# Kernel optimization log

Measured on AMD Instinct MI355X. Metric: run time of the kernel, lower is better.

Reference implementation:

```python
import jax, jax.numpy as jnp
import numpy as np

N = 50000
E = 800000
IN, HID, OUT = 64, 128, 64


def sage_conv(x, edge_index, W_l, b_l, W_r):
    # PyG SAGEConv (aggr='mean', root_weight=True):
    #   out = lin_l(mean_{j in N(i)} x_j) + lin_r(x_i)
    src, dst = edge_index[0], edge_index[1]
    msg = x[src]                                   # [E, d] gather
    agg = jax.ops.segment_sum(msg, dst, num_segments=x.shape[0])  # [N, d]
    cnt = jax.ops.segment_sum(jnp.ones((msg.shape[0],), x.dtype), dst,
                              num_segments=x.shape[0])
    mean = agg / jnp.maximum(cnt, 1.0)[:, None]
    return mean @ W_l + b_l + x @ W_r


def setup_inputs() -> dict:
    key = jax.random.key(0)
    ks = jax.random.split(key, 8)
    x = jax.random.normal(ks[0], (N, IN), dtype=jnp.float32)
    edge_index = jax.random.randint(ks[1], (2, E), 0, N, dtype=jnp.int64)
    s1 = 1.0 / np.sqrt(IN)
    s2 = 1.0 / np.sqrt(HID)
    W1_l = jax.random.uniform(ks[2], (IN, HID), jnp.float32, -s1, s1)
    W1_r = jax.random.uniform(ks[3], (IN, HID), jnp.float32, -s1, s1)
    b1 = jax.random.uniform(ks[4], (HID,), jnp.float32, -s1, s1)
    W2_l = jax.random.uniform(ks[5], (HID, OUT), jnp.float32, -s2, s2)
    W2_r = jax.random.uniform(ks[6], (HID, OUT), jnp.float32, -s2, s2)
    b2 = jax.random.uniform(ks[7], (OUT,), jnp.float32, -s2, s2)
    return {"x": x, "edge_index": edge_index,
            "W1_l": W1_l, "b1": b1, "W1_r": W1_r,
            "W2_l": W2_l, "b2": b2, "W2_r": W2_r}


def reference(x, edge_index, W1_l, b1, W1_r, W2_l, b2, W2_r):
    h = jax.nn.relu(sage_conv(x, edge_index, W1_l, b1, W1_r))
    return sage_conv(h, edge_index, W2_l, b2, W2_r)
```

## Files before the change

kernel.cpp:

```cpp
#include <hip/hip_runtime.h>


#define FMA4(acc, f, w0, w1, w2, w3)                          \
  acc.x += f.x * w0.x + f.y * w1.x + f.z * w2.x + f.w * w3.x; \
  acc.y += f.x * w0.y + f.y * w1.y + f.z * w2.y + f.w * w3.y; \
  acc.z += f.x * w0.z + f.y * w1.z + f.z * w2.z + f.w * w3.z; \
  acc.w += f.x * w0.w + f.y * w1.w + f.z * w2.w + f.w * w3.w;

__global__ __launch_bounds__(256) void k_hist(const int* __restrict__ dst,
                                              int* __restrict__ deg, int E) {
  int e = blockIdx.x * blockDim.x + threadIdx.x;
  if (e < E) atomicAdd(&deg[dst[e]], 1);
}

__global__ __launch_bounds__(256) void k_assign(const int* __restrict__ deg,
                                                int* __restrict__ rowptr,
                                                int* __restrict__ pos,
                                                int* __restrict__ total,
                                                int N) {
  int i = blockIdx.x * blockDim.x + threadIdx.x;
  if (i >= N) return;
  int r = atomicAdd(total, deg[i]);
  rowptr[i] = r;
  pos[i] = r;
}

__global__ __launch_bounds__(256) void k_fill(const int* __restrict__ src,
                                              const int* __restrict__ dst,
                                              int* __restrict__ pos,
                                              int* __restrict__ colsrc, int E) {
  int e = blockIdx.x * blockDim.x + threadIdx.x;
  if (e >= E) return;
  int slot = atomicAdd(&pos[dst[e]], 1);
  colsrc[slot] = src[e];
}

__global__ __launch_bounds__(256) void k_gather(
    const float* __restrict__ feat, const int* __restrict__ rowptr,
    const int* __restrict__ deg, const int* __restrict__ colsrc,
    const float* __restrict__ addsrc, const float* __restrict__ bias,
    float* __restrict__ dstbuf, int N) {
  int wave = threadIdx.x >> 6;
  int lane = threadIdx.x & 63;
  int node = blockIdx.x * 4 + wave;
  if (node >= N) return;
  int beg = rowptr[node];
  int d = deg[node];
  int end = beg + d;
  int eg = lane >> 4;
  int c4 = (lane & 15) << 2;
  float4 s0 = make_float4(0.f, 0.f, 0.f, 0.f);
  float4 s1 = s0;
  int e = beg + eg;
  for (; e + 4 < end; e += 8) {
    const float4 v0 =
        *reinterpret_cast<const float4*>(feat + (size_t)colsrc[e] * 64 + c4);
    const float4 v1 = *reinterpret_cast<const float4*>(
        feat + (size_t)colsrc[e + 4] * 64 + c4);
    s0.x += v0.x; s0.y += v0.y; s0.z += v0.z; s0.w += v0.w;
    s1.x += v1.x; s1.y += v1.y; s1.z += v1.z; s1.w += v1.w;
  }
  for (; e < end; e += 4) {
    const float4 v =
        *reinterpret_cast<const float4*>(feat + (size_t)colsrc[e] * 64 + c4);
    s0.x += v.x; s0.y += v.y; s0.z += v.z; s0.w += v.w;
  }
  s0.x += s1.x; s0.y += s1.y; s0.z += s1.z; s0.w += s1.w;
#pragma unroll
  for (int m = 16; m <= 32; m <<= 1) {
    s0.x += __shfl_xor(s0.x, m);
    s0.y += __shfl_xor(s0.y, m);
    s0.z += __shfl_xor(s0.z, m);
    s0.w += __shfl_xor(s0.w, m);
  }
  if (eg == 0) {
    float r = 1.f / fmaxf((float)d, 1.f);
    float4 o = make_float4(s0.x * r, s0.y * r, s0.z * r, s0.w * r);
    if (addsrc != nullptr) {
      float4 a = *(const float4*)&addsrc[(size_t)node * 64 + c4];
      float4 b = *(const float4*)&bias[c4];
      o.x += a.x + b.x;
      o.y += a.y + b.y;
      o.z += a.z + b.z;
      o.w += a.w + b.w;
    }
    *reinterpret_cast<float4*>(dstbuf + (size_t)node * 64 + c4) = o;
  }
}

__global__ __launch_bounds__(256) void k_dense1(
    const float* __restrict__ x, const float* __restrict__ mean1,
    const float* __restrict__ W1l, const float* __restrict__ b1,
    const float* __restrict__ W1r, const float* __restrict__ W2l,
    const float* __restrict__ W2r, float* __restrict__ p,
    float* __restrict__ q, int N) {
  int i0 = blockIdx.x * 32;
  int tid = threadIdx.x;
  __shared__ float smem[32 * 132];
  float(*ms)[64] = (float(*)[64])smem;
  float(*xs)[64] = (float(*)[64])(smem + 32 * 64);
  float(*hs)[132] = (float(*)[132])smem;

  for (int t = tid; t < 512; t += 256) {
    int n = t >> 4;
    int c4 = (t & 15) << 2;
    int node = i0 + n;
    float4 zm, zx;
    if (node < N) {
      zm = *(const float4*)&mean1[(size_t)node * 64 + c4];
      zx = *(const float4*)&x[(size_t)node * 64 + c4];
    } else {
      zm = make_float4(0.f, 0.f, 0.f, 0.f);
      zx = zm;
    }
    *(float4*)&ms[n][c4] = zm;
    *(float4*)&xs[n][c4] = zx;
  }
  __syncthreads();

  int jt = tid & 31;
  int j0 = jt << 2;
  int nt = tid >> 5;
  int n0 = nt << 2;
  float4 acc[4];
  {
    float4 bj = *(const float4*)&b1[j0];
    acc[0] = bj; acc[1] = bj; acc[2] = bj; acc[3] = bj;
  }
  for (int k0 = 0; k0 < 64; k0 += 4) {
    float4 wl[4], wr[4];
#pragma unroll
    for (int kk = 0; kk < 4; ++kk) {
      wl[kk] = *(const float4*)&W1l[(size_t)(k0 + kk) * 128 + j0];
      wr[kk] = *(const float4*)&W1r[(size_t)(k0 + kk) * 128 + j0];
    }
#pragma unroll
    for (int n = 0; n < 4; ++n) {
      float4 m4 = *(const float4*)&ms[n0 + n][k0];
      float4 x4 = *(const float4*)&xs[n0 + n][k0];
      FMA4(acc[n], m4, wl[0], wl[1], wl[2], wl[3]);
      FMA4(acc[n], x4, wr[0], wr[1], wr[2], wr[3]);
    }
  }
  __syncthreads();

#pragma unroll
  for (int n = 0; n < 4; ++n) {
    float4 v = acc[n];
    v.x = fmaxf(v.x, 0.f);
    v.y = fmaxf(v.y, 0.f);
    v.z = fmaxf(v.z, 0.f);
    v.w = fmaxf(v.w, 0.f);
    *(float4*)&hs[n0 + n][j0] = v;
  }
  __syncthreads();

  const float* W = (tid < 128) ? W2l : W2r;
  float* ob = (tid < 128) ? p : q;
  int t2 = tid & 127;
  int jj0 = (t2 & 15) << 2;
  int nn0 = (t2 >> 4) << 2;
  float4 pa[4];
  pa[0] = make_float4(0.f, 0.f, 0.f, 0.f);
  pa[1] = pa[0]; pa[2] = pa[0]; pa[3] = pa[0];
  for (int k0 = 0; k0 < 128; k0 += 4) {
    float4 w[4];
#pragma unroll
    for (int kk = 0; kk < 4; ++kk)
      w[kk] = *(const float4*)&W[(size_t)(k0 + kk) * 64 + jj0];
#pragma unroll
    for (int n = 0; n < 4; ++n) {
      float4 h4 = *(const float4*)&hs[nn0 + n][k0];
      FMA4(pa[n], h4, w[0], w[1], w[2], w[3]);
    }
  }
#pragma unroll
  for (int n = 0; n < 4; ++n) {
    int node = i0 + nn0 + n;
    if (node < N) *(float4*)&ob[(size_t)node * 64 + jj0] = pa[n];
  }
}

extern "C" void kernel_launch(void* const* d_in, const int* in_sizes, int n_in,
                              void* d_out, int out_size, void* d_ws,
                              size_t ws_size, hipStream_t stream) {
  const float* x = (const float*)d_in[0];
  const int* ei = (const int*)d_in[1];
  const float* W1l = (const float*)d_in[2];
  const float* b1 = (const float*)d_in[3];
  const float* W1r = (const float*)d_in[4];
  const float* W2l = (const float*)d_in[5];
  const float* b2 = (const float*)d_in[6];
  const float* W2r = (const float*)d_in[7];
  float* out = (float*)d_out;

  const int N = in_sizes[0] / 64;
  const int E = in_sizes[1] / 2;
  const int* src = ei;
  const int* dst = ei + E;

  int* deg = (int*)d_ws;
  int* total = deg + N;
  int* rowptr = total + 1;
  int* pos = rowptr + N;
  int* colsrc = pos + N;
  float* mean = (float*)(colsrc + E);
  float* p = mean + (size_t)N * 64;
  float* q = p + (size_t)N * 64;

  hipMemsetAsync(deg, 0, (size_t)(N + 1) * sizeof(int), stream);
  k_hist<<<(E + 255) / 256, 256, 0, stream>>>(dst, deg, E);
  k_assign<<<(N + 255) / 256, 256, 0, stream>>>(deg, rowptr, pos, total, N);
  k_fill<<<(E + 255) / 256, 256, 0, stream>>>(src, dst, pos, colsrc, E);

  int nblk4 = (N + 3) / 4;
  int nblk32 = (N + 31) / 32;
  k_gather<<<nblk4, 256, 0, stream>>>(x, rowptr, deg, colsrc, nullptr, nullptr,
                                      mean, N);
  k_dense1<<<nblk32, 256, 0, stream>>>(x, mean, W1l, b1, W1r, W2l, W2r, p, q,
                                       N);
  k_gather<<<nblk4, 256, 0, stream>>>(p, rowptr, deg, colsrc, q, b2, out, N);
}
```

Measured before the change: 324.7 us.

## Fuse layer-1 neighbor aggregation into dense kernel and unroll layer-2 gather

```diff
diff --git a/kernel.cpp b/kernel.cpp
--- a/kernel.cpp
+++ b/kernel.cpp
@@ -35,11 +35,145 @@
   colsrc[slot] = src[e];
 }
 
-__global__ __launch_bounds__(256) void k_gather(
-    const float* __restrict__ feat, const int* __restrict__ rowptr,
+__global__ __launch_bounds__(256, 4) void k_layer1(
+    const float* __restrict__ x, const int* __restrict__ rowptr,
     const int* __restrict__ deg, const int* __restrict__ colsrc,
-    const float* __restrict__ addsrc, const float* __restrict__ bias,
-    float* __restrict__ dstbuf, int N) {
+    const float* __restrict__ W1l, const float* __restrict__ b1,
+    const float* __restrict__ W1r, const float* __restrict__ W2l,
+    const float* __restrict__ W2r, float* __restrict__ p,
+    float* __restrict__ q, int N) {
+  int i0 = blockIdx.x * 32;
+  int tid = threadIdx.x;
+  __shared__ float smem[32 * 132];
+  float(*ms)[64] = (float(*)[64])smem;
+  float(*xs)[64] = (float(*)[64])(smem + 32 * 64);
+  float(*hs)[132] = (float(*)[132])smem;
+
+  {
+    int wv = tid >> 6;
+    int ln = tid & 63;
+    int eg = ln >> 4;
+    int c4 = (ln & 15) << 2;
+    for (int nn = 0; nn < 8; ++nn) {
+      int n = wv * 8 + nn;
+      int node = i0 + n;
+      float4 s0 = make_float4(0.f, 0.f, 0.f, 0.f);
+      float4 s1 = s0;
+      int d = 0;
+      if (node < N) {
+        int beg = rowptr[node];
+        d = deg[node];
+        int end = beg + d;
+        int e = beg + eg;
+        for (; e + 4 < end; e += 8) {
+          const float4 v0 = *reinterpret_cast<const float4*>(
+              x + (size_t)colsrc[e] * 64 + c4);
+          const float4 v1 = *reinterpret_cast<const float4*>(
+              x + (size_t)colsrc[e + 4] * 64 + c4);
+          s0.x += v0.x; s0.y += v0.y; s0.z += v0.z; s0.w += v0.w;
+          s1.x += v1.x; s1.y += v1.y; s1.z += v1.z; s1.w += v1.w;
+        }
+        for (; e < end; e += 4) {
+          const float4 v = *reinterpret_cast<const float4*>(
+              x + (size_t)colsrc[e] * 64 + c4);
+          s0.x += v.x; s0.y += v.y; s0.z += v.z; s0.w += v.w;
+        }
+      }
+      s0.x += s1.x; s0.y += s1.y; s0.z += s1.z; s0.w += s1.w;
+#pragma unroll
+      for (int m = 16; m <= 32; m <<= 1) {
+        s0.x += __shfl_xor(s0.x, m);
+        s0.y += __shfl_xor(s0.y, m);
+        s0.z += __shfl_xor(s0.z, m);
+        s0.w += __shfl_xor(s0.w, m);
+      }
+      if (eg == 0) {
+        float r = 1.f / fmaxf((float)d, 1.f);
+        *(float4*)&ms[n][c4] =
+            make_float4(s0.x * r, s0.y * r, s0.z * r, s0.w * r);
+      }
+    }
+  }
+  for (int t = tid; t < 512; t += 256) {
+    int n = t >> 4;
+    int c4 = (t & 15) << 2;
+    int node = i0 + n;
+    float4 zx = make_float4(0.f, 0.f, 0.f, 0.f);
+    if (node < N) zx = *(const float4*)&x[(size_t)node * 64 + c4];
+    *(float4*)&xs[n][c4] = zx;
+  }
+  __syncthreads();
+
+  int jt = tid & 31;
+  int j0 = jt << 2;
+  int nt = tid >> 5;
+  int n0 = nt << 2;
+  float4 acc[4];
+  {
+    float4 bj = *(const float4*)&b1[j0];
+    acc[0] = bj; acc[1] = bj; acc[2] = bj; acc[3] = bj;
+  }
+#pragma unroll 4
+  for (int k0 = 0; k0 < 64; k0 += 4) {
+    float4 wl[4], wr[4];
+#pragma unroll
+    for (int kk = 0; kk < 4; ++kk) {
+      wl[kk] = *(const float4*)&W1l[(size_t)(k0 + kk) * 128 + j0];
+      wr[kk] = *(const float4*)&W1r[(size_t)(k0 + kk) * 128 + j0];
+    }
+#pragma unroll
+    for (int n = 0; n < 4; ++n) {
+      float4 m4 = *(const float4*)&ms[n0 + n][k0];
+      float4 x4 = *(const float4*)&xs[n0 + n][k0];
+      FMA4(acc[n], m4, wl[0], wl[1], wl[2], wl[3]);
+      FMA4(acc[n], x4, wr[0], wr[1], wr[2], wr[3]);
+    }
+  }
+  __syncthreads();
+
+#pragma unroll
+  for (int n = 0; n < 4; ++n) {
+    float4 v = acc[n];
+    v.x = fmaxf(v.x, 0.f);
+    v.y = fmaxf(v.y, 0.f);
+    v.z = fmaxf(v.z, 0.f);
+    v.w = fmaxf(v.w, 0.f);
+    *(float4*)&hs[n0 + n][j0] = v;
+  }
+  __syncthreads();
+
+  const float* W = (tid < 128) ? W2l : W2r;
+  float* ob = (tid < 128) ? p : q;
+  int t2 = tid & 127;
+  int jj0 = (t2 & 15) << 2;
+  int nn0 = (t2 >> 4) << 2;
+  float4 pa[4];
+  pa[0] = make_float4(0.f, 0.f, 0.f, 0.f);
+  pa[1] = pa[0]; pa[2] = pa[0]; pa[3] = pa[0];
+#pragma unroll 4
+  for (int k0 = 0; k0 < 128; k0 += 4) {
+    float4 w[4];
+#pragma unroll
+    for (int kk = 0; kk < 4; ++kk)
+      w[kk] = *(const float4*)&W[(size_t)(k0 + kk) * 64 + jj0];
+#pragma unroll
+    for (int n = 0; n < 4; ++n) {
+      float4 h4 = *(const float4*)&hs[nn0 + n][k0];
+      FMA4(pa[n], h4, w[0], w[1], w[2], w[3]);
+    }
+  }
+#pragma unroll
+  for (int n = 0; n < 4; ++n) {
+    int node = i0 + nn0 + n;
+    if (node < N) *(float4*)&ob[(size_t)node * 64 + jj0] = pa[n];
+  }
+}
+
+__global__ __launch_bounds__(256) void k_layer2(
+    const float* __restrict__ p, const int* __restrict__ rowptr,
+    const int* __restrict__ deg, const int* __restrict__ colsrc,
+    const float* __restrict__ q, const float* __restrict__ b2,
+    float* __restrict__ out, int N) {
   int wave = threadIdx.x >> 6;
   int lane = threadIdx.x & 63;
   int node = blockIdx.x * 4 + wave;
@@ -50,22 +184,31 @@
   int eg = lane >> 4;
   int c4 = (lane & 15) << 2;
   float4 s0 = make_float4(0.f, 0.f, 0.f, 0.f);
-  float4 s1 = s0;
+  float4 s1 = s0, s2 = s0, s3 = s0;
   int e = beg + eg;
-  for (; e + 4 < end; e += 8) {
+  for (; e + 12 < end; e += 16) {
     const float4 v0 =
-        *reinterpret_cast<const float4*>(feat + (size_t)colsrc[e] * 64 + c4);
-    const float4 v1 = *reinterpret_cast<const float4*>(
-        feat + (size_t)colsrc[e + 4] * 64 + c4);
+        *reinterpret_cast<const float4*>(p + (size_t)colsrc[e] * 64 + c4);
+    const float4 v1 =
+        *reinterpret_cast<const float4*>(p + (size_t)colsrc[e + 4] * 64 + c4);
+    const float4 v2 =
+        *reinterpret_cast<const float4*>(p + (size_t)colsrc[e + 8] * 64 + c4);
+    const float4 v3 =
+        *reinterpret_cast<const float4*>(p + (size_t)colsrc[e + 12] * 64 + c4);
     s0.x += v0.x; s0.y += v0.y; s0.z += v0.z; s0.w += v0.w;
     s1.x += v1.x; s1.y += v1.y; s1.z += v1.z; s1.w += v1.w;
+    s2.x += v2.x; s2.y += v2.y; s2.z += v2.z; s2.w += v2.w;
+    s3.x += v3.x; s3.y += v3.y; s3.z += v3.z; s3.w += v3.w;
   }
   for (; e < end; e += 4) {
     const float4 v =
-        *reinterpret_cast<const float4*>(feat + (size_t)colsrc[e] * 64 + c4);
+        *reinterpret_cast<const float4*>(p + (size_t)colsrc[e] * 64 + c4);
     s0.x += v.x; s0.y += v.y; s0.z += v.z; s0.w += v.w;
   }
-  s0.x += s1.x; s0.y += s1.y; s0.z += s1.z; s0.w += s1.w;
+  s0.x += s1.x + s2.x + s3.x;
+  s0.y += s1.y + s2.y + s3.y;
+  s0.z += s1.z + s2.z + s3.z;
+  s0.w += s1.w + s2.w + s3.w;
 #pragma unroll
   for (int m = 16; m <= 32; m <<= 1) {
     s0.x += __shfl_xor(s0.x, m);
@@ -75,109 +218,11 @@
   }
   if (eg == 0) {
     float r = 1.f / fmaxf((float)d, 1.f);
-    float4 o = make_float4(s0.x * r, s0.y * r, s0.z * r, s0.w * r);
-    if (addsrc != nullptr) {
-      float4 a = *(const float4*)&addsrc[(size_t)node * 64 + c4];
-      float4 b = *(const float4*)&bias[c4];
-      o.x += a.x + b.x;
-      o.y += a.y + b.y;
-      o.z += a.z + b.z;
-      o.w += a.w + b.w;
-    }
-    *reinterpret_cast<float4*>(dstbuf + (size_t)node * 64 + c4) = o;
-  }
-}
-
-__global__ __launch_bounds__(256) void k_dense1(
-    const float* __restrict__ x, const float* __restrict__ mean1,
-    const float* __restrict__ W1l, const float* __restrict__ b1,
-    const float* __restrict__ W1r, const float* __restrict__ W2l,
-    const float* __restrict__ W2r, float* __restrict__ p,
-    float* __restrict__ q, int N) {
-  int i0 = blockIdx.x * 32;
-  int tid = threadIdx.x;
-  __shared__ float smem[32 * 132];
-  float(*ms)[64] = (float(*)[64])smem;
-  float(*xs)[64] = (float(*)[64])(smem + 32 * 64);
-  float(*hs)[132] = (float(*)[132])smem;
-
-  for (int t = tid; t < 512; t += 256) {
-    int n = t >> 4;
-    int c4 = (t & 15) << 2;
-    int node = i0 + n;
-    float4 zm, zx;
-    if (node < N) {
-      zm = *(const float4*)&mean1[(size_t)node * 64 + c4];
-      zx = *(const float4*)&x[(size_t)node * 64 + c4];
-    } else {
-      zm = make_float4(0.f, 0.f, 0.f, 0.f);
-      zx = zm;
-    }
-    *(float4*)&ms[n][c4] = zm;
-    *(float4*)&xs[n][c4] = zx;
-  }
-  __syncthreads();
-
-  int jt = tid & 31;
-  int j0 = jt << 2;
-  int nt = tid >> 5;
-  int n0 = nt << 2;
-  float4 acc[4];
-  {
-    float4 bj = *(const float4*)&b1[j0];
-    acc[0] = bj; acc[1] = bj; acc[2] = bj; acc[3] = bj;
-  }
-  for (int k0 = 0; k0 < 64; k0 += 4) {
-    float4 wl[4], wr[4];
-#pragma unroll
-    for (int kk = 0; kk < 4; ++kk) {
-      wl[kk] = *(const float4*)&W1l[(size_t)(k0 + kk) * 128 + j0];
-      wr[kk] = *(const float4*)&W1r[(size_t)(k0 + kk) * 128 + j0];
-    }
-#pragma unroll
-    for (int n = 0; n < 4; ++n) {
-      float4 m4 = *(const float4*)&ms[n0 + n][k0];
-      float4 x4 = *(const float4*)&xs[n0 + n][k0];
-      FMA4(acc[n], m4, wl[0], wl[1], wl[2], wl[3]);
-      FMA4(acc[n], x4, wr[0], wr[1], wr[2], wr[3]);
-    }
-  }
-  __syncthreads();
-
-#pragma unroll
-  for (int n = 0; n < 4; ++n) {
-    float4 v = acc[n];
-    v.x = fmaxf(v.x, 0.f);
-    v.y = fmaxf(v.y, 0.f);
-    v.z = fmaxf(v.z, 0.f);
-    v.w = fmaxf(v.w, 0.f);
-    *(float4*)&hs[n0 + n][j0] = v;
-  }
-  __syncthreads();
-
-  const float* W = (tid < 128) ? W2l : W2r;
-  float* ob = (tid < 128) ? p : q;
-  int t2 = tid & 127;
-  int jj0 = (t2 & 15) << 2;
-  int nn0 = (t2 >> 4) << 2;
-  float4 pa[4];
-  pa[0] = make_float4(0.f, 0.f, 0.f, 0.f);
-  pa[1] = pa[0]; pa[2] = pa[0]; pa[3] = pa[0];
-  for (int k0 = 0; k0 < 128; k0 += 4) {
-    float4 w[4];
-#pragma unroll
-    for (int kk = 0; kk < 4; ++kk)
-      w[kk] = *(const float4*)&W[(size_t)(k0 + kk) * 64 + jj0];
-#pragma unroll
-    for (int n = 0; n < 4; ++n) {
-      float4 h4 = *(const float4*)&hs[nn0 + n][k0];
-      FMA4(pa[n], h4, w[0], w[1], w[2], w[3]);
-    }
-  }
-#pragma unroll
-  for (int n = 0; n < 4; ++n) {
-    int node = i0 + nn0 + n;
-    if (node < N) *(float4*)&ob[(size_t)node * 64 + jj0] = pa[n];
+    float4 a = *(const float4*)&q[(size_t)node * 64 + c4];
+    float4 b = *(const float4*)&b2[c4];
+    float4 o = make_float4(s0.x * r + a.x + b.x, s0.y * r + a.y + b.y,
+                           s0.z * r + a.z + b.z, s0.w * r + a.w + b.w);
+    *reinterpret_cast<float4*>(out + (size_t)node * 64 + c4) = o;
   }
 }
 
@@ -204,8 +249,7 @@
   int* rowptr = total + 1;
   int* pos = rowptr + N;
   int* colsrc = pos + N;
-  float* mean = (float*)(colsrc + E);
-  float* p = mean + (size_t)N * 64;
+  float* p = (float*)(colsrc + E);
   float* q = p + (size_t)N * 64;
 
   hipMemsetAsync(deg, 0, (size_t)(N + 1) * sizeof(int), stream);
@@ -213,11 +257,9 @@
   k_assign<<<(N + 255) / 256, 256, 0, stream>>>(deg, rowptr, pos, total, N);
   k_fill<<<(E + 255) / 256, 256, 0, stream>>>(src, dst, pos, colsrc, E);
 
+  int nblk32 = (N + 31) / 32;
   int nblk4 = (N + 3) / 4;
-  int nblk32 = (N + 31) / 32;
-  k_gather<<<nblk4, 256, 0, stream>>>(x, rowptr, deg, colsrc, nullptr, nullptr,
-                                      mean, N);
-  k_dense1<<<nblk32, 256, 0, stream>>>(x, mean, W1l, b1, W1r, W2l, W2r, p, q,
-                                       N);
-  k_gather<<<nblk4, 256, 0, stream>>>(p, rowptr, deg, colsrc, q, b2, out, N);
-}
+  k_layer1<<<nblk32, 256, 0, stream>>>(x, rowptr, deg, colsrc, W1l, b1, W1r,
+                                       W2l, W2r, p, q, N);
+  k_layer2<<<nblk4, 256, 0, stream>>>(p, rowptr, deg, colsrc, q, b2, out, N);
+}
```

Result: no change. 327.4 us (+0.8%).
